# Kernel tuning notes

Hardware: AMD Instinct MI355X
Metric: run time of the kernel (lower is better)

The kernel has to match this reference:

```python
import jax, jax.numpy as jnp
import numpy as np

NUM_USERS = 100000
NUM_ITEMS = 100000
N = NUM_USERS + NUM_ITEMS
D = 64
E = 3200000


def setup_inputs() -> dict:
    key = jax.random.key(0)
    ks = jax.random.split(key, 8)
    edge_index = jax.random.randint(ks[0], (2, E), 0, N, dtype=jnp.int64)
    edge_weight = jax.random.uniform(ks[1], (E,), dtype=jnp.float32)
    user_emb = jax.random.normal(ks[2], (NUM_USERS, D), dtype=jnp.float32) * 0.1
    item_emb = jax.random.normal(ks[3], (NUM_ITEMS, D), dtype=jnp.float32) * 0.1
    s = 1.0 / np.sqrt(D)
    W1 = jax.random.uniform(ks[4], (D, D), dtype=jnp.float32, minval=-s, maxval=s)
    b1 = jax.random.uniform(ks[5], (D,), dtype=jnp.float32, minval=-s, maxval=s)
    W2 = jax.random.uniform(ks[6], (D, D), dtype=jnp.float32, minval=-s, maxval=s)
    b2 = jax.random.uniform(ks[7], (D,), dtype=jnp.float32, minval=-s, maxval=s)
    return {"edge_index": edge_index, "edge_weight": edge_weight,
            "user_emb": user_emb, "item_emb": item_emb,
            "W1": W1, "b1": b1, "W2": W2, "b2": b2}


def _gcn_layer(x, src, dst, edge_weight, W, b):
    # message: edge_weight * x[src]; aggregate: scatter-add at dst
    msg = edge_weight[:, None] * x[src]              # [E, D] gather + mul
    agg = jax.ops.segment_sum(msg, dst, num_segments=N)  # [N, D] scatter-add
    updated = (agg + x) * 0.5                        # residual average
    return updated @ W + b                           # linear


def reference(edge_index, edge_weight, user_emb, item_emb, W1, b1, W2, b2):
    src = edge_index[0]
    dst = edge_index[1]
    x = jnp.concatenate([user_emb, item_emb], axis=0)  # [N, D]
    x = _gcn_layer(x, src, dst, edge_weight, W1, b1)
    x = _gcn_layer(x, src, dst, edge_weight, W2, b2)
    return x
```

## Files before the change

kernel.cpp:

```cpp
#include <hip/hip_runtime.h>
#include <hip/hip_fp16.h>

#define NUM_USERS 100000
#define NN        200000
#define DD        64
#define EE        3200000
#define SCAN_CHUNK 2048
#define NB_SCAN   98

#define KB_   391
#define GSEG  512
#define EPS   (EE / GSEG)
#define MSEG  (KB_ * GSEG)

typedef _Float16 half8 __attribute__((ext_vector_type(8)));
typedef _Float16 half4 __attribute__((ext_vector_type(4)));
typedef float    f32x4 __attribute__((ext_vector_type(4)));

__global__ __launch_bounds__(256) void scan_partials_kernel(
    const int* __restrict__ counts, int* __restrict__ bsum, int len)
{
    __shared__ int s[256];
    const int t = threadIdx.x;
    int sum = 0;
    for (int i = t; i < SCAN_CHUNK; i += 256) {
        const int idx = blockIdx.x * SCAN_CHUNK + i;
        sum += (idx < len) ? counts[idx] : 0;
    }
    s[t] = sum; __syncthreads();
    for (int off = 128; off > 0; off >>= 1) {
        if (t < off) s[t] += s[t + off];
        __syncthreads();
    }
    if (t == 0) bsum[blockIdx.x] = s[0];
}

__global__ __launch_bounds__(128) void scan_top_kernel(int* __restrict__ bsum, int nb)
{
    __shared__ int s[128];
    const int t = threadIdx.x;
    const int v = (t < nb) ? bsum[t] : 0;
    s[t] = v; __syncthreads();
    for (int off = 1; off < 128; off <<= 1) {
        int add = (t >= off) ? s[t - off] : 0;
        __syncthreads();
        s[t] += add;
        __syncthreads();
    }
    if (t < nb) bsum[t] = s[t] - v;
}

__global__ __launch_bounds__(256) void scan_write_kernel(
    const int* __restrict__ counts, const int* __restrict__ bsum,
    int* __restrict__ out, int len)
{
    __shared__ int s[256];
    const int t    = threadIdx.x;
    const int base = blockIdx.x * SCAN_CHUNK + t * 8;
    int c[8], ex[8], run = 0;
#pragma unroll
    for (int j = 0; j < 8; ++j) {
        const int idx = base + j;
        c[j] = (idx < len) ? counts[idx] : 0;
        ex[j] = run; run += c[j];
    }
    s[t] = run; __syncthreads();
    for (int off = 1; off < 256; off <<= 1) {
        int add = (t >= off) ? s[t - off] : 0;
        __syncthreads();
        s[t] += add;
        __syncthreads();
    }
    const int thread_base = bsum[blockIdx.x] + s[t] - run;
#pragma unroll
    for (int j = 0; j < 8; ++j) {
        const int idx = base + j;
        if (idx < len) out[idx] = thread_base + ex[j];
    }
}

__global__ __launch_bounds__(256) void seg_hist_kernel(
    const int* __restrict__ ei, int* __restrict__ counts_seg)
{
    __shared__ int h[KB_];
    const int s = blockIdx.x;
    for (int k = threadIdx.x; k < KB_; k += 256) h[k] = 0;
    __syncthreads();
    const int base = s * EPS;
    for (int i = threadIdx.x; i < EPS; i += 256) {
        const int dst = __builtin_nontemporal_load(&ei[EE + base + i]);
        atomicAdd(&h[dst >> 9], 1);
    }
    __syncthreads();
    for (int k = threadIdx.x; k < KB_; k += 256)
        counts_seg[k * GSEG + s] = h[k];
}

__global__ __launch_bounds__(256) void append_kernel(
    const int* __restrict__ ei, const float* __restrict__ ew,
    const int* __restrict__ bofs, int2* __restrict__ etmp)
{
    __shared__ int fr[KB_];
    const int s = blockIdx.x;
    for (int k = threadIdx.x; k < KB_; k += 256) fr[k] = bofs[k * GSEG + s];
    __syncthreads();
    const int base = s * EPS;
    for (int i = threadIdx.x; i < EPS; i += 256) {
        const int e   = base + i;
        const int   src = __builtin_nontemporal_load(&ei[e]);
        const int   dst = __builtin_nontemporal_load(&ei[EE + e]);
        const float w   = __builtin_nontemporal_load(&ew[e]);
        const int k  = dst >> 9;
        const int dl = dst & 511;
        const int pos = atomicAdd(&fr[k], 1);
        etmp[pos] = make_int2(src | (dl << 18), __float_as_int(w));
    }
}

__global__ __launch_bounds__(256) void bucket_sort_kernel(
    const int2* __restrict__ etmp, const int* __restrict__ bofs,
    int2* __restrict__ edges, int* __restrict__ row_ptr)
{
    __shared__ int cnt[512];
    __shared__ int cur[512];
    __shared__ int part[256];
    const int k = blockIdx.x;
    const int t = threadIdx.x;
    cnt[t] = 0; cnt[t + 256] = 0;
    __syncthreads();
    const int beg = bofs[k * GSEG];
    const int end = (k == KB_ - 1) ? EE : bofs[(k + 1) * GSEG];
    for (int e = beg + t; e < end; e += 256)
        atomicAdd(&cnt[((unsigned)etmp[e].x) >> 18], 1);
    __syncthreads();
    const int c0 = cnt[2 * t], c1 = cnt[2 * t + 1];
    const int run = c0 + c1;
    part[t] = run; __syncthreads();
    for (int off = 1; off < 256; off <<= 1) {
        int add = (t >= off) ? part[t - off] : 0;
        __syncthreads();
        part[t] += add;
        __syncthreads();
    }
    const int base = beg + part[t] - run;
    cur[2 * t]     = base;
    cur[2 * t + 1] = base + c0;
    const int node0 = (k << 9) + 2 * t;
    if (node0 < NN)     row_ptr[node0]     = base;
    if (node0 + 1 < NN) row_ptr[node0 + 1] = base + c0;
    if (k == KB_ - 1 && t == 0) row_ptr[NN] = EE;
    __syncthreads();
    for (int e = beg + t; e < end; e += 256) {
        const int2 r  = etmp[e];
        const int  dl = ((unsigned)r.x) >> 18;
        const int  pos = atomicAdd(&cur[dl], 1);
        edges[pos] = make_int2((r.x & 0x3FFFF) << 7, r.y);
    }
}

__global__ __launch_bounds__(256) void convert_x_kernel(
    const float* __restrict__ xu, const float* __restrict__ xi,
    _Float16* __restrict__ xh)
{
    const int i = blockIdx.x * 256 + threadIdx.x;
    if (i >= NN * DD / 4) return;
    const float4 v = (i < NUM_USERS * DD / 4)
                       ? ((const float4*)xu)[i]
                       : ((const float4*)xi)[i - NUM_USERS * DD / 4];
    half4 o; o[0] = (_Float16)v.x; o[1] = (_Float16)v.y;
             o[2] = (_Float16)v.z; o[3] = (_Float16)v.w;
    ((half4*)xh)[i] = o;
}

__global__ __launch_bounds__(256) void convert_w_kernel(
    const float* __restrict__ W1, const float* __restrict__ W2,
    _Float16* __restrict__ Wt)
{
    const int idx = blockIdx.x * 256 + threadIdx.x;
    if (idx >= 2 * DD * DD) return;
    const int mat = idx >> 12, rem = idx & 4095, k = rem >> 6, n = rem & 63;
    const float* W = mat ? W2 : W1;
    Wt[mat * DD * DD + n * DD + k] = (_Float16)W[k * DD + n];
}

__global__ __launch_bounds__(256) void aggregate_kernel(
    const int2* __restrict__ edges, const int* __restrict__ row_ptr,
    const _Float16* __restrict__ xh, _Float16* __restrict__ u)
{
    const int wave = (blockIdx.x * 256 + threadIdx.x) >> 6;
    const int lane = threadIdx.x & 63;
    const unsigned lane2 = lane * 2;
    const int nbase = wave * 4;
    const char* xb = (const char*)xh;

    int e0 = __builtin_amdgcn_readfirstlane(row_ptr[nbase + 0]);
    const int f0 = __builtin_amdgcn_readfirstlane(row_ptr[nbase + 1]);
    const int f1 = __builtin_amdgcn_readfirstlane(row_ptr[nbase + 2]);
    const int f2 = __builtin_amdgcn_readfirstlane(row_ptr[nbase + 3]);
    const int f3 = __builtin_amdgcn_readfirstlane(row_ptr[nbase + 4]);
    int e1 = f0, e2 = f1, e3 = f2;

    float acc0 = (float)*(const _Float16*)(xb + ((unsigned)(nbase + 0) << 7) + lane2);
    float acc1 = (float)*(const _Float16*)(xb + ((unsigned)(nbase + 1) << 7) + lane2);
    float acc2 = (float)*(const _Float16*)(xb + ((unsigned)(nbase + 2) << 7) + lane2);
    float acc3 = (float)*(const _Float16*)(xb + ((unsigned)(nbase + 3) << 7) + lane2);

    while ((e0 < f0) || (e1 < f1) || (e2 < f2) || (e3 < f3)) {
        int2  rec[16];
        float wv[16];
        _Float16 hv[16];

#pragma unroll
        for (int j = 0; j < 4; ++j) {
            int idx = e0 + j;
            const bool ok = idx < f0;
            idx = ok ? idx : f0 - 1;
            idx = idx > 0 ? idx : 0;
            rec[j] = edges[idx];
            hv[j] = *(const _Float16*)(xb + (unsigned)rec[j].x + lane2);
            wv[j] = ok ? __int_as_float(rec[j].y) : 0.0f;
        }
#pragma unroll
        for (int j = 0; j < 4; ++j) {
            int idx = e1 + j;
            const bool ok = idx < f1;
            idx = ok ? idx : f1 - 1;
            idx = idx > 0 ? idx : 0;
            rec[4 + j] = edges[idx];
            hv[4 + j] = *(const _Float16*)(xb + (unsigned)rec[4 + j].x + lane2);
            wv[4 + j] = ok ? __int_as_float(rec[4 + j].y) : 0.0f;
        }
#pragma unroll
        for (int j = 0; j < 4; ++j) {
            int idx = e2 + j;
            const bool ok = idx < f2;
            idx = ok ? idx : f2 - 1;
            idx = idx > 0 ? idx : 0;
            rec[8 + j] = edges[idx];
            hv[8 + j] = *(const _Float16*)(xb + (unsigned)rec[8 + j].x + lane2);
            wv[8 + j] = ok ? __int_as_float(rec[8 + j].y) : 0.0f;
        }
#pragma unroll
        for (int j = 0; j < 4; ++j) {
            int idx = e3 + j;
            const bool ok = idx < f3;
            idx = ok ? idx : f3 - 1;
            idx = idx > 0 ? idx : 0;
            rec[12 + j] = edges[idx];
            hv[12 + j] = *(const _Float16*)(xb + (unsigned)rec[12 + j].x + lane2);
            wv[12 + j] = ok ? __int_as_float(rec[12 + j].y) : 0.0f;
        }

#pragma unroll
        for (int j = 0; j < 4; ++j) acc0 = fmaf(wv[j],      (float)hv[j],      acc0);
#pragma unroll
        for (int j = 0; j < 4; ++j) acc1 = fmaf(wv[4 + j],  (float)hv[4 + j],  acc1);
#pragma unroll
        for (int j = 0; j < 4; ++j) acc2 = fmaf(wv[8 + j],  (float)hv[8 + j],  acc2);
#pragma unroll
        for (int j = 0; j < 4; ++j) acc3 = fmaf(wv[12 + j], (float)hv[12 + j], acc3);

        e0 += 4; e1 += 4; e2 += 4; e3 += 4;
    }

    char* ub = (char*)u;
    *(_Float16*)(ub + ((unsigned)(nbase + 0) << 7) + lane2) = (_Float16)(acc0 * 0.5f);
    *(_Float16*)(ub + ((unsigned)(nbase + 1) << 7) + lane2) = (_Float16)(acc1 * 0.5f);
    *(_Float16*)(ub + ((unsigned)(nbase + 2) << 7) + lane2) = (_Float16)(acc2 * 0.5f);
    *(_Float16*)(ub + ((unsigned)(nbase + 3) << 7) + lane2) = (_Float16)(acc3 * 0.5f);
}

template<bool HALF_OUT>
__global__ __launch_bounds__(256) void gemm64_kernel(
    const _Float16* __restrict__ u, const _Float16* __restrict__ Wt,
    const float* __restrict__ bias, void* __restrict__ outp)
{
    const int wid  = blockIdx.x * 4 + (threadIdx.x >> 6);
    const int lane = threadIdx.x & 63;
    const int m    = lane & 15;
    const int quad = lane >> 4;
    const size_t rowbase = (size_t)wid * 16;

    half8 bf[4][2];
#pragma unroll
    for (int c = 0; c < 4; ++c)
#pragma unroll
        for (int h = 0; h < 2; ++h)
            bf[c][h] = *(const half8*)(Wt + (size_t)(c * 16 + m) * DD + h * 32 + quad * 8);

    const half8 a0 = *(const half8*)(u + (rowbase + m) * DD +  0 + quad * 8);
    const half8 a1 = *(const half8*)(u + (rowbase + m) * DD + 32 + quad * 8);

    f32x4 acc[4];
#pragma unroll
    for (int c = 0; c < 4; ++c) {
        f32x4 z = {0.f, 0.f, 0.f, 0.f};
        z = __builtin_amdgcn_mfma_f32_16x16x32_f16(a0, bf[c][0], z, 0, 0, 0);
        z = __builtin_amdgcn_mfma_f32_16x16x32_f16(a1, bf[c][1], z, 0, 0, 0);
        acc[c] = z;
    }

#pragma unroll
    for (int c = 0; c < 4; ++c) {
        const float bv = bias[c * 16 + m];
#pragma unroll
        for (int r = 0; r < 4; ++r) {
            const size_t row = rowbase + quad * 4 + r;
            const float val = acc[c][r] + bv;
            if (HALF_OUT) ((_Float16*)outp)[row * DD + c * 16 + m] = (_Float16)val;
            else          ((float*)    outp)[row * DD + c * 16 + m] = val;
        }
    }
}

extern "C" void kernel_launch(void* const* d_in, const int* in_sizes, int n_in,
                              void* d_out, int out_size, void* d_ws, size_t ws_size,
                              hipStream_t stream) {
    const int*   edge_index  = (const int*)  d_in[0];
    const float* edge_weight = (const float*)d_in[1];
    const float* user_emb    = (const float*)d_in[2];
    const float* item_emb    = (const float*)d_in[3];
    const float* W1          = (const float*)d_in[4];
    const float* b1          = (const float*)d_in[5];
    const float* W2          = (const float*)d_in[6];
    const float* b2          = (const float*)d_in[7];
    float*       out         = (float*)d_out;

    char* ws = (char*)d_ws;
    _Float16* xh        = (_Float16*)(ws);
    _Float16* u         = (_Float16*)(ws + 25600000);
    int2*     etmp      = (int2*)    (ws + 25600000);
    int2*     edges     = (int2*)    (ws + 51200000);
    int*      row_ptr   = (int*)     (ws + 76800000);
    int*      cseg      = (int*)     (ws + 78400064);
    int*      bofs      = (int*)     (ws + 79200832);
    int*      bsum      = (int*)     (ws + 80001600);
    _Float16* Wt        = (_Float16*)(ws + 80002112);

    const int gemm_blocks = (NN / 16) / 4;
    const int agg_blocks  = NN / 16;

    seg_hist_kernel     <<<GSEG,    256, 0, stream>>>(edge_index, cseg);
    scan_partials_kernel<<<NB_SCAN, 256, 0, stream>>>(cseg, bsum, MSEG);
    scan_top_kernel     <<<1,       128, 0, stream>>>(bsum, NB_SCAN);
    scan_write_kernel   <<<NB_SCAN, 256, 0, stream>>>(cseg, bsum, bofs, MSEG);

    append_kernel      <<<GSEG, 256, 0, stream>>>(edge_index, edge_weight, bofs, etmp);
    bucket_sort_kernel <<<KB_,  256, 0, stream>>>(etmp, bofs, edges, row_ptr);

    convert_x_kernel<<<(NN * DD / 4 + 255) / 256, 256, 0, stream>>>(user_emb, item_emb, xh);
    convert_w_kernel<<<(2 * DD * DD + 255) / 256, 256, 0, stream>>>(W1, W2, Wt);

    aggregate_kernel<<<agg_blocks, 256, 0, stream>>>(edges, row_ptr, xh, u);
    gemm64_kernel<true><<<gemm_blocks, 256, 0, stream>>>(u, Wt, b1, (void*)xh);

    aggregate_kernel<<<agg_blocks, 256, 0, stream>>>(edges, row_ptr, xh, u);
    gemm64_kernel<false><<<gemm_blocks, 256, 0, stream>>>(u, Wt + DD * DD, b2, (void*)out);
}
```

Baseline: 518.0 us.

## Split wave into quarter-waves per node with half4 vector gathers

Reassigns lanes in the CSR aggregation kernel so that each 16-lane quarter of a wave handles one of the four destination nodes, with each lane owning four contiguous feature columns loaded as a half4. Previously every lane loaded a single fp16 element for all four nodes, issuing 16 scalar-width gathers per iteration. Now each lane issues 4 wider gathers and does 4 FMAs per edge. This cuts the number of memory instructions and makes each gather 8 bytes wide. The cost is that every lane still loads all four edge records and selects its own, and the loop runs until the longest of the four node lists is done.

```diff
diff --git a/kernel.cpp b/kernel.cpp
--- a/kernel.cpp
+++ b/kernel.cpp
@@ -189,8 +189,10 @@
 {
     const int wave = (blockIdx.x * 256 + threadIdx.x) >> 6;
     const int lane = threadIdx.x & 63;
-    const unsigned lane2 = lane * 2;
     const int nbase = wave * 4;
+    const int q    = lane >> 4;
+    const int i16  = lane & 15;
+    const unsigned qoff = (unsigned)i16 * 8;
     const char* xb = (const char*)xh;
 
     int e0 = __builtin_amdgcn_readfirstlane(row_ptr[nbase + 0]);
@@ -200,74 +202,53 @@
     const int f3 = __builtin_amdgcn_readfirstlane(row_ptr[nbase + 4]);
     int e1 = f0, e2 = f1, e3 = f2;
 
-    float acc0 = (float)*(const _Float16*)(xb + ((unsigned)(nbase + 0) << 7) + lane2);
-    float acc1 = (float)*(const _Float16*)(xb + ((unsigned)(nbase + 1) << 7) + lane2);
-    float acc2 = (float)*(const _Float16*)(xb + ((unsigned)(nbase + 2) << 7) + lane2);
-    float acc3 = (float)*(const _Float16*)(xb + ((unsigned)(nbase + 3) << 7) + lane2);
-
-    while ((e0 < f0) || (e1 < f1) || (e2 < f2) || (e3 < f3)) {
-        int2  rec[16];
-        float wv[16];
-        _Float16 hv[16];
-
+    const unsigned rowb = ((unsigned)(nbase + q)) << 7;
+    const half4 xi = *(const half4*)(xb + rowb + qoff);
+    float a0 = (float)xi[0], a1 = (float)xi[1];
+    float a2 = (float)xi[2], a3 = (float)xi[3];
+
+    const bool lo32 = lane < 32;
+    const bool loq  = (lane & 16) == 0;
+
+    while ((e0 < f0) | (e1 < f1) | (e2 < f2) | (e3 < f3)) {
+        int   bx[4];
+        float ww[4];
+        half4 hv[4];
 #pragma unroll
         for (int j = 0; j < 4; ++j) {
-            int idx = e0 + j;
-            const bool ok = idx < f0;
-            idx = ok ? idx : f0 - 1;
-            idx = idx > 0 ? idx : 0;
-            rec[j] = edges[idx];
-            hv[j] = *(const _Float16*)(xb + (unsigned)rec[j].x + lane2);
-            wv[j] = ok ? __int_as_float(rec[j].y) : 0.0f;
+            int i0 = e0 + j; const bool k0 = i0 < f0; i0 = k0 ? i0 : f0 - 1; i0 = i0 > 0 ? i0 : 0;
+            int i1 = e1 + j; const bool k1 = i1 < f1; i1 = k1 ? i1 : f1 - 1; i1 = i1 > 0 ? i1 : 0;
+            int i2 = e2 + j; const bool k2 = i2 < f2; i2 = k2 ? i2 : f2 - 1; i2 = i2 > 0 ? i2 : 0;
+            int i3 = e3 + j; const bool k3 = i3 < f3; i3 = k3 ? i3 : f3 - 1; i3 = i3 > 0 ? i3 : 0;
+            const int2 r0 = edges[i0];
+            const int2 r1 = edges[i1];
+            const int2 r2 = edges[i2];
+            const int2 r3 = edges[i3];
+            const float w0 = k0 ? __int_as_float(r0.y) : 0.0f;
+            const float w1 = k1 ? __int_as_float(r1.y) : 0.0f;
+            const float w2 = k2 ? __int_as_float(r2.y) : 0.0f;
+            const float w3 = k3 ? __int_as_float(r3.y) : 0.0f;
+            bx[j] = lo32 ? (loq ? r0.x : r1.x) : (loq ? r2.x : r3.x);
+            ww[j] = lo32 ? (loq ? w0 : w1) : (loq ? w2 : w3);
+            hv[j] = *(const half4*)(xb + (unsigned)bx[j] + qoff);
         }
 #pragma unroll
         for (int j = 0; j < 4; ++j) {
-            int idx = e1 + j;
-            const bool ok = idx < f1;
-            idx = ok ? idx : f1 - 1;
-            idx = idx > 0 ? idx : 0;
-            rec[4 + j] = edges[idx];
-            hv[4 + j] = *(const _Float16*)(xb + (unsigned)rec[4 + j].x + lane2);
-            wv[4 + j] = ok ? __int_as_float(rec[4 + j].y) : 0.0f;
+            a0 = fmaf(ww[j], (float)hv[j][0], a0);
+            a1 = fmaf(ww[j], (float)hv[j][1], a1);
+            a2 = fmaf(ww[j], (float)hv[j][2], a2);
+            a3 = fmaf(ww[j], (float)hv[j][3], a3);
         }
-#pragma unroll
-        for (int j = 0; j < 4; ++j) {
-            int idx = e2 + j;
-            const bool ok = idx < f2;
-            idx = ok ? idx : f2 - 1;
-            idx = idx > 0 ? idx : 0;
-            rec[8 + j] = edges[idx];
-            hv[8 + j] = *(const _Float16*)(xb + (unsigned)rec[8 + j].x + lane2);
-            wv[8 + j] = ok ? __int_as_float(rec[8 + j].y) : 0.0f;
-        }
-#pragma unroll
-        for (int j = 0; j < 4; ++j) {
-            int idx = e3 + j;
-            const bool ok = idx < f3;
-            idx = ok ? idx : f3 - 1;
-            idx = idx > 0 ? idx : 0;
-            rec[12 + j] = edges[idx];
-            hv[12 + j] = *(const _Float16*)(xb + (unsigned)rec[12 + j].x + lane2);
-            wv[12 + j] = ok ? __int_as_float(rec[12 + j].y) : 0.0f;
-        }
-
-#pragma unroll
-        for (int j = 0; j < 4; ++j) acc0 = fmaf(wv[j],      (float)hv[j],      acc0);
-#pragma unroll
-        for (int j = 0; j < 4; ++j) acc1 = fmaf(wv[4 + j],  (float)hv[4 + j],  acc1);
-#pragma unroll
-        for (int j = 0; j < 4; ++j) acc2 = fmaf(wv[8 + j],  (float)hv[8 + j],  acc2);
-#pragma unroll
-        for (int j = 0; j < 4; ++j) acc3 = fmaf(wv[12 + j], (float)hv[12 + j], acc3);
-
         e0 += 4; e1 += 4; e2 += 4; e3 += 4;
     }
 
     char* ub = (char*)u;
-    *(_Float16*)(ub + ((unsigned)(nbase + 0) << 7) + lane2) = (_Float16)(acc0 * 0.5f);
-    *(_Float16*)(ub + ((unsigned)(nbase + 1) << 7) + lane2) = (_Float16)(acc1 * 0.5f);
-    *(_Float16*)(ub + ((unsigned)(nbase + 2) << 7) + lane2) = (_Float16)(acc2 * 0.5f);
-    *(_Float16*)(ub + ((unsigned)(nbase + 3) << 7) + lane2) = (_Float16)(acc3 * 0.5f);
+    half4 o;
+    o[0] = (_Float16)(a0 * 0.5f);
+    o[1] = (_Float16)(a1 * 0.5f);
+    o[2] = (_Float16)(a2 * 0.5f);
+    o[3] = (_Float16)(a3 * 0.5f);
+    *(half4*)(ub + rowb + qoff) = o;
 }
 
 template<bool HALF_OUT>
```

New measurement: 499.6 us. 3.6% less time.
